# Kernel optimization log

Hardware: AMD Instinct MI355X
Metric: run time of the kernel (lower is better)

## Reference

```python
import jax, jax.numpy as jnp
import numpy as np

DIM, NH, T_MAX = 1024, 16, 2048
HD = DIM // NH
EPS = 1e-6


def _rope_tables(T, hd, dtype=jnp.float32):
    inv_freq = 1.0 / (10000.0 ** (jnp.arange(0, hd, 2, dtype=jnp.float32) / hd))
    t = jnp.arange(T, dtype=jnp.float32)
    freqs = jnp.outer(t, inv_freq)                 # [T, hd/2]
    emb = jnp.concatenate([freqs, freqs], axis=-1)  # [T, hd]
    return jnp.cos(emb).astype(dtype), jnp.sin(emb).astype(dtype)


def _rotate_half(x):
    x1, x2 = jnp.split(x, 2, axis=-1)
    return jnp.concatenate([-x2, x1], axis=-1)


def _rmsnorm(x, g):
    rms = jnp.sqrt(jnp.mean(x * x, axis=-1, keepdims=True) + EPS)
    return x / rms * g


def setup_inputs() -> dict:
    key = jax.random.key(0)
    ks = jax.random.split(key, 10)
    B, T, C = 4, 2048, DIM
    s = 1.0 / np.sqrt(C)
    x = jax.random.normal(ks[0], (B, T, C), dtype=jnp.float32)
    mask = jnp.tril(jnp.ones((T, T), dtype=jnp.int32))[None, None, :, :]
    wq = jax.random.normal(ks[1], (C, C), jnp.float32) * s
    wk = jax.random.normal(ks[2], (C, C), jnp.float32) * s
    wv = jax.random.normal(ks[3], (C, C), jnp.float32) * s
    wo = jax.random.normal(ks[4], (C, C), jnp.float32) * s
    w1 = jax.random.normal(ks[5], (C, 4 * C), jnp.float32) * s
    w2 = jax.random.normal(ks[6], (4 * C, C), jnp.float32) * (1.0 / np.sqrt(4 * C))
    w3 = jax.random.normal(ks[7], (C, 4 * C), jnp.float32) * s
    g1 = jnp.ones((C,), jnp.float32)
    g2 = jnp.ones((C,), jnp.float32)
    return {"x": x, "mask": mask, "g1": g1, "wq": wq, "wk": wk, "wv": wv,
            "wo": wo, "g2": g2, "w1": w1, "w2": w2, "w3": w3}


def reference(x, mask, g1, wq, wk, wv, wo, g2, w1, w2, w3):
    B, T, C = x.shape
    scale = HD ** -0.5
    # --- attention sublayer ---
    h = _rmsnorm(x, g1)
    q = (h @ wq).reshape(B, T, NH, HD)
    k = (h @ wk).reshape(B, T, NH, HD)
    v = (h @ wv).reshape(B, T, NH, HD)
    cos, sin = _rope_tables(T, HD, x.dtype)
    cos = cos[None, :, None, :]
    sin = sin[None, :, None, :]
    q = q * cos + _rotate_half(q) * sin
    k = k * cos + _rotate_half(k) * sin
    attn = jnp.einsum("bthd,bshd->bhts", q, k) * scale  # [B,H,T,T]
    attn = jnp.where(mask == 0, -jnp.inf, attn)
    attn = jax.nn.softmax(attn, axis=-1)
    o = jnp.einsum("bhts,bshd->bthd", attn, v).reshape(B, T, C)
    x = x + o @ wo
    # --- SwiGLU FFN sublayer ---
    h = _rmsnorm(x, g2)
    x = x + (jax.nn.silu(h @ w1) * (h @ w3)) @ w2
    return x
```

## Files before the change

kernel.cpp:

```cpp
#include <hip/hip_runtime.h>
#include <cstdint>

typedef unsigned short u16;
typedef __attribute__((ext_vector_type(8))) short bf16x8;
typedef __attribute__((ext_vector_type(4))) float f32x4;

__device__ __forceinline__ u16 f2b(float f) {
  union { float f; unsigned u; } c; c.f = f;
  unsigned u = c.u;
  return (u16)((u + 0x7FFFu + ((u >> 16) & 1u)) >> 16);
}
__device__ __forceinline__ float b2f(u16 b) {
  union { unsigned u; float f; } c; c.u = ((unsigned)b) << 16;
  return c.f;
}

typedef __attribute__((address_space(1))) void gv_t;
typedef __attribute__((address_space(3))) void lv_t;
__device__ __forceinline__ void gload_lds16(const void* g, void* l) {
  __builtin_amdgcn_global_load_lds((gv_t*)g, (lv_t*)l, 16, 0, 0);
}

__global__ void transpose_f2b(const float* __restrict__ in, u16* __restrict__ out,
                              int R, int C) {
  __shared__ float t[32][33];
  const int c0 = blockIdx.x * 32, r0 = blockIdx.y * 32;
  const int tx = threadIdx.x, ty = threadIdx.y;
#pragma unroll
  for (int i = 0; i < 4; ++i)
    t[ty + 8 * i][tx] = in[(size_t)(r0 + ty + 8 * i) * C + c0 + tx];
  __syncthreads();
#pragma unroll
  for (int i = 0; i < 4; ++i)
    out[(size_t)(c0 + ty + 8 * i) * R + r0 + tx] = f2b(t[tx][ty + 8 * i]);
}

__global__ __launch_bounds__(256) void rmsnorm_k(const float* __restrict__ x,
                                                 const float* __restrict__ g,
                                                 u16* __restrict__ out) {
  const int row = blockIdx.x, tid = threadIdx.x;
  const float4 v = ((const float4*)x)[(size_t)row * 256 + tid];
  float ss = v.x * v.x + v.y * v.y + v.z * v.z + v.w * v.w;
#pragma unroll
  for (int off = 1; off < 64; off <<= 1) ss += __shfl_xor(ss, off, 64);
  __shared__ float red[4];
  if ((tid & 63) == 0) red[tid >> 6] = ss;
  __syncthreads();
  const float mean = (red[0] + red[1] + red[2] + red[3]) * (1.0f / 1024.0f);
  const float rinv = 1.0f / sqrtf(mean + 1e-6f);
  const float4 gv = ((const float4*)g)[tid];
  u16* o = out + (size_t)row * 1024 + tid * 4;
  o[0] = f2b(v.x * rinv * gv.x);
  o[1] = f2b(v.y * rinv * gv.y);
  o[2] = f2b(v.z * rinv * gv.z);
  o[3] = f2b(v.w * rinv * gv.w);
}

__global__ __launch_bounds__(256) void rope_k(u16* __restrict__ qkv) {
  const int i = blockIdx.x * 256 + threadIdx.x;
  const int d = i & 31;
  const int h = (i >> 5) & 15;
  const int bt = i >> 9;
  const int t = bt & 2047;
  const float inv = exp2f((float)d * -0.4152410118609203f);
  const float th = (float)t * inv;
  float s, c;
  sincosf(th, &s, &c);
  size_t base = (size_t)bt * 3072 + h * 64 + d;
#pragma unroll
  for (int half = 0; half < 2; ++half) {
    const float x1 = b2f(qkv[base]);
    const float x2 = b2f(qkv[base + 32]);
    qkv[base]      = f2b(x1 * c - x2 * s);
    qkv[base + 32] = f2b(x2 * c + x1 * s);
    base += 1024;
  }
}

__global__ void vtrans_k(const u16* __restrict__ qkv, u16* __restrict__ VT) {
  __shared__ u16 tl[32][34];
  const int t0 = blockIdx.x * 32;
  const int bh = blockIdx.y >> 1;
  const int d0 = (blockIdx.y & 1) * 32;
  const int b = bh >> 4, h = bh & 15;
  const int tx = threadIdx.x, ty = threadIdx.y;
  const u16* src = qkv + (size_t)(b * 2048 + t0) * 3072 + 2048 + h * 64 + d0;
#pragma unroll
  for (int i = 0; i < 4; ++i)
    tl[ty + 8 * i][tx] = src[(size_t)(ty + 8 * i) * 3072 + tx];
  __syncthreads();
  u16* dst = VT + ((size_t)bh * 64 + d0) * 2048 + t0;
#pragma unroll
  for (int i = 0; i < 4; ++i)
    dst[(size_t)(ty + 8 * i) * 2048 + tx] = tl[tx][ty + 8 * i];
}

template <int EPI>
__global__ __launch_bounds__(512, 2)
void gemm256(const u16* __restrict__ A, const u16* __restrict__ BT,
             void* __restrict__ Cout, const float* __restrict__ resid,
             int M, int N, int K, int lda) {
  __shared__ alignas(16) u16 LDS[65536];
  char* const ldsc = (char*)LDS;
  const int tid = threadIdx.x;
  const int wave = tid >> 6, lane = tid & 63;
  const int wr = wave >> 2, wc = wave & 3;
  const int l15 = lane & 15, quad = lane >> 4;
  const int bm = blockIdx.x * 256, bn = blockIdx.y * 256;
  const int NT = K >> 6;

  const int swz = (l15 & 8) << 2;
  const int aoff = (((wr * 64 + l15) * 64 + quad * 16) ^ swz);
  const int boff = (((wc * 32 + l15) * 64 + quad * 16) ^ swz) + 65536;

  const int kperm = ((lane & 3) ^ ((lane >> 5) << 1)) * 8;
  const u16* sA = A + (size_t)(bm + wave * 16 + (lane >> 2)) * lda + kperm;
  const u16* sB = BT + (size_t)(bn + wave * 16 + (lane >> 2)) * K + kperm;
  const size_t hA = (size_t)128 * lda;
  const size_t hB = (size_t)128 * K;
  const int dstW = wave * 1024;

  f32x4 acc[8][4];
#pragma unroll
  for (int m = 0; m < 8; ++m)
#pragma unroll
    for (int n = 0; n < 4; ++n) acc[m][n] = (f32x4){0.f, 0.f, 0.f, 0.f};
  bf16x8 a[4][2], b[4][2];

#define STAGE(kt_, slot_, buf_)                                               \
  if ((kt_) < NT) {                                                           \
    const u16* s_ = (((slot_) & 1) ? sB + ((size_t)((slot_) >> 1)) * hB       \
                                   : sA + ((size_t)((slot_) >> 1)) * hA) +    \
                    (size_t)(kt_) * 64;                                       \
    char* d_ = ldsc + (((slot_) & 1) ? 65536 : 0) + (buf_) * 32768 +          \
               ((slot_) >> 1) * 16384 + dstW;                                 \
    gload_lds16(s_, d_);                                                      \
    gload_lds16(s_ + 32, d_ + 8192);                                          \
  }

#define LOAD_A(mh_, buf_)                                                     \
  _Pragma("unroll") for (int mf = 0; mf < 4; ++mf)                            \
      _Pragma("unroll") for (int kk = 0; kk < 2; ++kk)                        \
          a[mf][kk] = *(const bf16x8*)(ldsc + aoff + (buf_) * 32768 +         \
                                       (mh_) * 16384 + kk * 8192 + mf * 1024);

#define LOAD_B2(buf_)                                                         \
  _Pragma("unroll") for (int nh = 0; nh < 2; ++nh)                            \
      _Pragma("unroll") for (int nf = 0; nf < 2; ++nf)                        \
          _Pragma("unroll") for (int kk = 0; kk < 2; ++kk)                    \
              b[nh * 2 + nf][kk] =                                            \
                  *(const bf16x8*)(ldsc + boff + (buf_) * 32768 +             \
                                   nh * 16384 + kk * 8192 + nf * 1024);

#define MMA2(mh_)                                                             \
  __builtin_amdgcn_s_setprio(1);                                              \
  _Pragma("unroll") for (int mf = 0; mf < 4; ++mf)                            \
      _Pragma("unroll") for (int n = 0; n < 4; ++n)                           \
          _Pragma("unroll") for (int kk = 0; kk < 2; ++kk)                    \
              acc[(mh_) * 4 + mf][n] =                                        \
                  __builtin_amdgcn_mfma_f32_16x16x32_bf16(                    \
                      a[mf][kk], b[n][kk], acc[(mh_) * 4 + mf][n], 0, 0, 0);  \
  __builtin_amdgcn_s_setprio(0);

#define BAR() __builtin_amdgcn_s_barrier()
#define DRAIN_LGKM()                                                          \
  {                                                                           \
    asm volatile("s_waitcnt lgkmcnt(0)" ::: "memory");                        \
    __builtin_amdgcn_sched_barrier(0);                                        \
  }

  STAGE(0, 0, 0); STAGE(0, 1, 0); STAGE(0, 3, 0);
  STAGE(0, 2, 0);
  STAGE(1, 0, 1); STAGE(1, 1, 1); STAGE(1, 3, 1);
  asm volatile("s_waitcnt vmcnt(8)" ::: "memory");
  BAR();

  for (int t = 0; t < NT; ++t) {
    const int bsel = t & 1;
    LOAD_A(0, bsel); LOAD_B2(bsel);
    STAGE(t + 1, 2, bsel ^ 1);
    BAR(); DRAIN_LGKM(); MMA2(0);
    if (t == NT - 1) { asm volatile("s_waitcnt vmcnt(0)" ::: "memory"); }
    else             { asm volatile("s_waitcnt vmcnt(8)" ::: "memory"); }
    BAR();
    LOAD_A(1, bsel);
    STAGE(t + 2, 0, bsel); STAGE(t + 2, 1, bsel); STAGE(t + 2, 3, bsel);
    BAR(); DRAIN_LGKM(); MMA2(1);
    if (t < NT - 2) {
      asm volatile("s_waitcnt vmcnt(8)" ::: "memory");
      BAR();
    } else if (t == NT - 2) {
      asm volatile("s_waitcnt vmcnt(2)" ::: "memory");
      BAR();
    }
  }
#undef STAGE
#undef LOAD_A
#undef LOAD_B2
#undef MMA2

#pragma unroll
  for (int m = 0; m < 8; ++m) {
    const int gr = bm + (m >> 2) * 128 + wr * 64 + (m & 3) * 16 + quad * 4;
#pragma unroll
    for (int n = 0; n < 4; ++n) {
      const int gc = bn + (n >> 1) * 128 + wc * 32 + (n & 1) * 16 + l15;
#pragma unroll
      for (int r = 0; r < 4; ++r) {
        const size_t off = (size_t)(gr + r) * N + gc;
        if (EPI == 0) {
          ((u16*)Cout)[off] = f2b(acc[m][n][r]);
        } else {
          ((float*)Cout)[off] = resid[off] + acc[m][n][r];
        }
      }
    }
  }
#undef BAR
#undef DRAIN_LGKM
}

__global__ __launch_bounds__(512, 2)
void gemm256g(const u16* __restrict__ A, const u16* __restrict__ B1T,
              const u16* __restrict__ B3T, u16* __restrict__ Cout,
              int Ncols, int K, int lda) {
  __shared__ alignas(16) u16 LDS[65536];
  char* const ldsc = (char*)LDS;
  const int tid = threadIdx.x;
  const int wave = tid >> 6, lane = tid & 63;
  const int wr = wave >> 2, wc = wave & 3;
  const int l15 = lane & 15, quad = lane >> 4;
  const int bm = blockIdx.x * 256, bn = blockIdx.y * 128;
  const int NT = K >> 6;

  const int swz = (l15 & 8) << 2;
  const int aoff  = (((wr * 64 + l15) * 64 + quad * 16) ^ swz);
  const int b1off = (((wc * 32 + l15) * 64 + quad * 16) ^ swz) + 65536;

  const int kperm = ((lane & 3) ^ ((lane >> 5) << 1)) * 8;
  const u16* sA  = A   + (size_t)(bm + wave * 16 + (lane >> 2)) * lda + kperm;
  const u16* sB1 = B1T + (size_t)(bn + wave * 16 + (lane >> 2)) * K + kperm;
  const u16* sB3 = B3T + (size_t)(bn + wave * 16 + (lane >> 2)) * K + kperm;
  const size_t hA = (size_t)128 * lda;
  const int dstW = wave * 1024;

  f32x4 acc1[8][2], acc3[8][2];
#pragma unroll
  for (int m = 0; m < 8; ++m)
#pragma unroll
    for (int n = 0; n < 2; ++n) {
      acc1[m][n] = (f32x4){0.f, 0.f, 0.f, 0.f};
      acc3[m][n] = (f32x4){0.f, 0.f, 0.f, 0.f};
    }
  bf16x8 a[4][2], b1[2][2], b3[2][2];

#define STAGE_A(kt_, half_, buf_)                                             \
  if ((kt_) < NT) {                                                           \
    const u16* s_ = sA + (size_t)(half_) * hA + (size_t)(kt_) * 64;           \
    char* d_ = ldsc + (buf_) * 32768 + (half_) * 16384 + dstW;                \
    gload_lds16(s_, d_);                                                      \
    gload_lds16(s_ + 32, d_ + 8192);                                          \
  }
#define STAGE_B1(kt_, buf_)                                                   \
  if ((kt_) < NT) {                                                           \
    const u16* s_ = sB1 + (size_t)(kt_) * 64;                                 \
    char* d_ = ldsc + 65536 + (buf_) * 16384 + dstW;                          \
    gload_lds16(s_, d_);                                                      \
    gload_lds16(s_ + 32, d_ + 8192);                                          \
  }
#define STAGE_B3(kt_, buf_)                                                   \
  if ((kt_) < NT) {                                                           \
    const u16* s_ = sB3 + (size_t)(kt_) * 64;                                 \
    char* d_ = ldsc + 98304 + (buf_) * 16384 + dstW;                          \
    gload_lds16(s_, d_);                                                      \
    gload_lds16(s_ + 32, d_ + 8192);                                          \
  }
#define LOAD_A(mh_, buf_)                                                     \
  _Pragma("unroll") for (int mf = 0; mf < 4; ++mf)                            \
      _Pragma("unroll") for (int kk = 0; kk < 2; ++kk)                        \
          a[mf][kk] = *(const bf16x8*)(ldsc + aoff + (buf_) * 32768 +         \
                                       (mh_) * 16384 + kk * 8192 + mf * 1024);
#define LOAD_B13(buf_)                                                        \
  _Pragma("unroll") for (int nf = 0; nf < 2; ++nf)                            \
      _Pragma("unroll") for (int kk = 0; kk < 2; ++kk) {                      \
        b1[nf][kk] = *(const bf16x8*)(ldsc + b1off + (buf_) * 16384 +         \
                                      kk * 8192 + nf * 1024);                 \
        b3[nf][kk] = *(const bf16x8*)(ldsc + b1off + 32768 +                  \
                                      (buf_) * 16384 + kk * 8192 +            \
                                      nf * 1024);                             \
      }
#define MMAG(mh_)                                                             \
  __builtin_amdgcn_s_setprio(1);                                              \
  _Pragma("unroll") for (int mf = 0; mf < 4; ++mf)                            \
      _Pragma("unroll") for (int nf = 0; nf < 2; ++nf)                        \
          _Pragma("unroll") for (int kk = 0; kk < 2; ++kk) {                  \
            acc1[(mh_) * 4 + mf][nf] =                                        \
                __builtin_amdgcn_mfma_f32_16x16x32_bf16(                      \
                    a[mf][kk], b1[nf][kk], acc1[(mh_) * 4 + mf][nf], 0, 0, 0);\
            acc3[(mh_) * 4 + mf][nf] =                                        \
                __builtin_amdgcn_mfma_f32_16x16x32_bf16(                      \
                    a[mf][kk], b3[nf][kk], acc3[(mh_) * 4 + mf][nf], 0, 0, 0);\
          }                                                                   \
  __builtin_amdgcn_s_setprio(0);
#define BAR() __builtin_amdgcn_s_barrier()
#define DRAIN_LGKM()                                                          \
  {                                                                           \
    asm volatile("s_waitcnt lgkmcnt(0)" ::: "memory");                        \
    __builtin_amdgcn_sched_barrier(0);                                        \
  }

  STAGE_A(0, 0, 0); STAGE_B1(0, 0); STAGE_B3(0, 0);
  STAGE_A(0, 1, 0);
  STAGE_A(1, 0, 1); STAGE_B1(1, 1); STAGE_B3(1, 1);
  asm volatile("s_waitcnt vmcnt(8)" ::: "memory");
  BAR();

  for (int t = 0; t < NT; ++t) {
    const int bsel = t & 1;
    LOAD_A(0, bsel); LOAD_B13(bsel);
    STAGE_A(t + 1, 1, bsel ^ 1);
    BAR(); DRAIN_LGKM(); MMAG(0);
    if (t == NT - 1) { asm volatile("s_waitcnt vmcnt(0)" ::: "memory"); }
    else             { asm volatile("s_waitcnt vmcnt(8)" ::: "memory"); }
    BAR();
    LOAD_A(1, bsel);
    STAGE_A(t + 2, 0, bsel); STAGE_B1(t + 2, bsel); STAGE_B3(t + 2, bsel);
    BAR(); DRAIN_LGKM(); MMAG(1);
    if (t < NT - 2) {
      asm volatile("s_waitcnt vmcnt(8)" ::: "memory");
      BAR();
    } else if (t == NT - 2) {
      asm volatile("s_waitcnt vmcnt(2)" ::: "memory");
      BAR();
    }
  }
#undef STAGE_A
#undef STAGE_B1
#undef STAGE_B3
#undef LOAD_A
#undef LOAD_B13
#undef MMAG
#undef BAR
#undef DRAIN_LGKM

#pragma unroll
  for (int m = 0; m < 8; ++m) {
    const int gr = bm + (m >> 2) * 128 + wr * 64 + (m & 3) * 16 + quad * 4;
#pragma unroll
    for (int n = 0; n < 2; ++n) {
      const int gc = bn + wc * 32 + n * 16 + l15;
#pragma unroll
      for (int r = 0; r < 4; ++r) {
        const float v1 = acc1[m][n][r];
        const float v3 = acc3[m][n][r];
        const float s = v1 / (1.f + __expf(-v1));
        Cout[(size_t)(gr + r) * Ncols + gc] = f2b(s * v3);
      }
    }
  }
}

template <int EPI>
__global__ __launch_bounds__(512, 2)
void gemm256n(const u16* __restrict__ A, const u16* __restrict__ BT,
              void* __restrict__ Cout, const float* __restrict__ resid,
              int M, int N, int K, int lda) {
  __shared__ alignas(16) u16 LDS[49152];
  char* const ldsc = (char*)LDS;
  const int tid = threadIdx.x;
  const int wave = tid >> 6, lane = tid & 63;
  const int wr = wave >> 2, wc = wave & 3;
  const int l15 = lane & 15, quad = lane >> 4;
  const int bm = blockIdx.x * 256, bn = blockIdx.y * 128;
  const int NT = K >> 6;

  const int swz = (l15 & 8) << 2;
  const int aoff = (((wr * 64 + l15) * 64 + quad * 16) ^ swz);
  const int boff = (((wc * 32 + l15) * 64 + quad * 16) ^ swz) + 65536;

  const int kperm = ((lane & 3) ^ ((lane >> 5) << 1)) * 8;
  const u16* sA = A + (size_t)(bm + wave * 16 + (lane >> 2)) * lda + kperm;
  const u16* sB = BT + (size_t)(bn + wave * 16 + (lane >> 2)) * K + kperm;
  const size_t hA = (size_t)128 * lda;
  const int dstW = wave * 1024;

  f32x4 acc[8][2];
#pragma unroll
  for (int m = 0; m < 8; ++m)
#pragma unroll
    for (int n = 0; n < 2; ++n) acc[m][n] = (f32x4){0.f, 0.f, 0.f, 0.f};
  bf16x8 a[4][2], b[2][2];

#define STAGE_A(kt_, half_, buf_)                                             \
  if ((kt_) < NT) {                                                           \
    const u16* s_ = sA + (size_t)(half_) * hA + (size_t)(kt_) * 64;           \
    char* d_ = ldsc + (buf_) * 32768 + (half_) * 16384 + dstW;                \
    gload_lds16(s_, d_);                                                      \
    gload_lds16(s_ + 32, d_ + 8192);                                          \
  }
#define STAGE_B(kt_, buf_)                                                    \
  if ((kt_) < NT) {                                                           \
    const u16* s_ = sB + (size_t)(kt_) * 64;                                  \
    char* d_ = ldsc + 65536 + (buf_) * 16384 + dstW;                          \
    gload_lds16(s_, d_);                                                      \
    gload_lds16(s_ + 32, d_ + 8192);                                          \
  }
#define LOAD_A(mh_, buf_)                                                     \
  _Pragma("unroll") for (int mf = 0; mf < 4; ++mf)                            \
      _Pragma("unroll") for (int kk = 0; kk < 2; ++kk)                        \
          a[mf][kk] = *(const bf16x8*)(ldsc + aoff + (buf_) * 32768 +         \
                                       (mh_) * 16384 + kk * 8192 + mf * 1024);
#define LOAD_B(buf_)                                                          \
  _Pragma("unroll") for (int nf = 0; nf < 2; ++nf)                            \
      _Pragma("unroll") for (int kk = 0; kk < 2; ++kk)                        \
          b[nf][kk] = *(const bf16x8*)(ldsc + boff + (buf_) * 16384 +         \
                                       kk * 8192 + nf * 1024);
#define MMA(mh_)                                                              \
  __builtin_amdgcn_s_setprio(1);                                              \
  _Pragma("unroll") for (int mf = 0; mf < 4; ++mf)                            \
      _Pragma("unroll") for (int nf = 0; nf < 2; ++nf)                        \
          _Pragma("unroll") for (int kk = 0; kk < 2; ++kk)                    \
              acc[(mh_) * 4 + mf][nf] =                                       \
                  __builtin_amdgcn_mfma_f32_16x16x32_bf16(                    \
                      a[mf][kk], b[nf][kk], acc[(mh_) * 4 + mf][nf], 0, 0, 0);\
  __builtin_amdgcn_s_setprio(0);
#define BAR() __builtin_amdgcn_s_barrier()
#define DRAIN_LGKM()                                                          \
  {                                                                           \
    asm volatile("s_waitcnt lgkmcnt(0)" ::: "memory");                        \
    __builtin_amdgcn_sched_barrier(0);                                        \
  }

  STAGE_A(0, 0, 0); STAGE_B(0, 0);
  STAGE_A(0, 1, 0);
  STAGE_A(1, 0, 1); STAGE_B(1, 1);
  asm volatile("s_waitcnt vmcnt(6)" ::: "memory");
  BAR();

  for (int t = 0; t < NT; ++t) {
    const int bsel = t & 1;
    LOAD_A(0, bsel); LOAD_B(bsel);
    STAGE_A(t + 1, 1, bsel ^ 1);
    BAR(); DRAIN_LGKM(); MMA(0);
    if (t == NT - 1) { asm volatile("s_waitcnt vmcnt(0)" ::: "memory"); }
    else             { asm volatile("s_waitcnt vmcnt(6)" ::: "memory"); }
    BAR();
    LOAD_A(1, bsel);
    STAGE_A(t + 2, 0, bsel); STAGE_B(t + 2, bsel);
    BAR(); DRAIN_LGKM(); MMA(1);
    if (t == NT - 2)     { asm volatile("s_waitcnt vmcnt(2)" ::: "memory"); }
    else if (t < NT - 2) { asm volatile("s_waitcnt vmcnt(6)" ::: "memory"); }
    BAR();
  }
#undef STAGE_A
#undef STAGE_B
#undef LOAD_A
#undef LOAD_B
#undef MMA
#undef BAR
#undef DRAIN_LGKM

#pragma unroll
  for (int m = 0; m < 8; ++m) {
    const int gr = bm + (m >> 2) * 128 + wr * 64 + (m & 3) * 16 + quad * 4;
#pragma unroll
    for (int n = 0; n < 2; ++n) {
      const int gc = bn + wc * 32 + n * 16 + l15;
#pragma unroll
      for (int r = 0; r < 4; ++r) {
        const size_t off = (size_t)(gr + r) * N + gc;
        if (EPI == 0) {
          ((u16*)Cout)[off] = f2b(acc[m][n][r]);
        } else {
          ((float*)Cout)[off] = resid[off] + acc[m][n][r];
        }
      }
    }
  }
}

__global__ __launch_bounds__(256)
void attn_kernel(const u16* __restrict__ QKV, const u16* __restrict__ VT,
                 u16* __restrict__ O, float* __restrict__ Opart,
                 float* __restrict__ Spart) {
  const int T = 2048, stQ = 3072;
  const int tid = threadIdx.x, wave = tid >> 6, lane = tid & 63;
  const int l15 = lane & 15, quad = lane >> 4;

  const int xi = (int)blockIdx.x;
  const bool split = (xi < 22);
  const int qt = split ? (15 - (xi >> 1)) : (26 - xi);
  const int chunk = split ? (xi & 1) : 0;
  const int len = split ? (qt + 1) : (2 * qt + 2);
  const int kt0 = chunk * (qt + 1);
  const int ktEnd = kt0 + len;

  const int qb0 = qt * 128;
  const int bh = blockIdx.y, b = bh >> 4, h = bh & 15;
  const float sc2 = 0.125f * 1.44269504088896f;
  const float M0 = 32.0f;

  __shared__ alignas(16) u16 Kf[2][8 * 512];
  __shared__ alignas(16) u16 Vf[2][8 * 512];
  __shared__ alignas(16) u16 Pl[4][2][16 * 72];

  const u16* Qb  = QKV + (size_t)b * T * stQ + h * 64;
  const u16* Kb  = Qb + 1024;
  const u16* VTb = VT + (size_t)bh * 64 * T;

  const int r0 = qb0 + wave * 16;
  const int r1 = r0 + 64;
  const u16* qp0 = Qb + (size_t)(r0 + l15) * stQ + quad * 8;
  const u16* qp1 = Qb + (size_t)(r1 + l15) * stQ + quad * 8;
  const bf16x8 qf00 = *(const bf16x8*)qp0;
  const bf16x8 qf01 = *(const bf16x8*)(qp0 + 32);
  const bf16x8 qf10 = *(const bf16x8*)qp1;
  const bf16x8 qf11 = *(const bf16x8*)(qp1 + 32);

  bf16x8 ones;
#pragma unroll
  for (int j = 0; j < 8; ++j) ones[j] = (short)0x3F80;

  const u16* kS = Kb + (size_t)(wave * 16 + l15) * stQ + quad * 8;
  const u16* vS = VTb + (size_t)(wave * 16 + l15) * T + quad * 8;

  f32x4 o0[4], o1[4], sum0, sum1;
#pragma unroll
  for (int c = 0; c < 4; ++c) {
    o0[c] = (f32x4){0.f, 0.f, 0.f, 0.f};
    o1[c] = (f32x4){0.f, 0.f, 0.f, 0.f};
  }
  sum0 = (f32x4){0.f, 0.f, 0.f, 0.f};
  sum1 = (f32x4){0.f, 0.f, 0.f, 0.f};

  u16* pw0 = &Pl[wave][0][0];
  u16* pw1 = &Pl[wave][1][0];

  gload_lds16(kS + (size_t)(kt0 * 64) * stQ,      &Kf[0][(wave * 2 + 0) * 512]);
  gload_lds16(kS + (size_t)(kt0 * 64) * stQ + 32, &Kf[0][(wave * 2 + 1) * 512]);
  gload_lds16(vS + (size_t)(kt0 * 64),            &Vf[0][(wave * 2 + 0) * 512]);
  gload_lds16(vS + (size_t)(kt0 * 64) + 32,       &Vf[0][(wave * 2 + 1) * 512]);

  for (int kt = kt0; kt < ktEnd; ++kt) {
    const int kb0 = kt * 64;
    const int buf = (kt - kt0) & 1;
    __builtin_amdgcn_sched_barrier(0);
    if (kt + 1 < ktEnd) {
      const size_t kb1 = (size_t)(kb0 + 64);
      gload_lds16(kS + kb1 * stQ,      &Kf[buf ^ 1][(wave * 2 + 0) * 512]);
      gload_lds16(kS + kb1 * stQ + 32, &Kf[buf ^ 1][(wave * 2 + 1) * 512]);
      gload_lds16(vS + kb1,            &Vf[buf ^ 1][(wave * 2 + 0) * 512]);
      gload_lds16(vS + kb1 + 32,       &Vf[buf ^ 1][(wave * 2 + 1) * 512]);
      asm volatile("s_waitcnt vmcnt(4)" ::: "memory");
    } else {
      asm volatile("s_waitcnt vmcnt(0)" ::: "memory");
    }
    __builtin_amdgcn_s_barrier();
    __builtin_amdgcn_sched_barrier(0);

    bf16x8 kf[8], vf[8];
#pragma unroll
    for (int g = 0; g < 8; ++g) {
      kf[g] = *(const bf16x8*)(&Kf[buf][g * 512 + lane * 8]);
      vf[g] = *(const bf16x8*)(&Vf[buf][g * 512 + lane * 8]);
    }

    const bool act0 = (kb0 <= r0 + 15);

    {
      f32x4 s[4];
      __builtin_amdgcn_s_setprio(1);
#pragma unroll
      for (int jj = 0; jj < 4; ++jj) {
        s[jj] = (f32x4){0.f, 0.f, 0.f, 0.f};
        s[jj] = __builtin_amdgcn_mfma_f32_16x16x32_bf16(qf10, kf[jj * 2 + 0], s[jj], 0, 0, 0);
        s[jj] = __builtin_amdgcn_mfma_f32_16x16x32_bf16(qf11, kf[jj * 2 + 1], s[jj], 0, 0, 0);
      }
      __builtin_amdgcn_s_setprio(0);
      if (kb0 + 63 > r1) {
#pragma unroll
        for (int jj = 0; jj < 4; ++jj)
#pragma unroll
          for (int r = 0; r < 4; ++r) {
            const bool msk = (kb0 + jj * 16 + l15) > (r1 + quad * 4 + r);
            const float a = msk ? -1e30f : (s[jj][r] * sc2 - M0);
            pw1[(quad * 4 + r) * 72 + jj * 16 + l15] = f2b(exp2f(a));
          }
      } else {
#pragma unroll
        for (int jj = 0; jj < 4; ++jj)
#pragma unroll
          for (int r = 0; r < 4; ++r)
            pw1[(quad * 4 + r) * 72 + jj * 16 + l15] =
                f2b(exp2f(s[jj][r] * sc2 - M0));
      }
    }
    if (act0) {
      f32x4 s[4];
      __builtin_amdgcn_s_setprio(1);
#pragma unroll
      for (int jj = 0; jj < 4; ++jj) {
        s[jj] = (f32x4){0.f, 0.f, 0.f, 0.f};
        s[jj] = __builtin_amdgcn_mfma_f32_16x16x32_bf16(qf00, kf[jj * 2 + 0], s[jj], 0, 0, 0);
        s[jj] = __builtin_amdgcn_mfma_f32_16x16x32_bf16(qf01, kf[jj * 2 + 1], s[jj], 0, 0, 0);
      }
      __builtin_amdgcn_s_setprio(0);
      if (kb0 + 63 > r0) {
#pragma unroll
        for (int jj = 0; jj < 4; ++jj)
#pragma unroll
          for (int r = 0; r < 4; ++r) {
            const bool msk = (kb0 + jj * 16 + l15) > (r0 + quad * 4 + r);
            const float a = msk ? -1e30f : (s[jj][r] * sc2 - M0);
            pw0[(quad * 4 + r) * 72 + jj * 16 + l15] = f2b(exp2f(a));
          }
      } else {
#pragma unroll
        for (int jj = 0; jj < 4; ++jj)
#pragma unroll
          for (int r = 0; r < 4; ++r)
            pw0[(quad * 4 + r) * 72 + jj * 16 + l15] =
                f2b(exp2f(s[jj][r] * sc2 - M0));
      }
    }

    const bf16x8 pf10 = *(const bf16x8*)(pw1 + l15 * 72 + quad * 8);
    const bf16x8 pf11 = *(const bf16x8*)(pw1 + l15 * 72 + 32 + quad * 8);
    __builtin_amdgcn_s_setprio(1);
#pragma unroll
    for (int c = 0; c < 4; ++c) {
      o1[c] = __builtin_amdgcn_mfma_f32_16x16x32_bf16(pf10, vf[c * 2 + 0], o1[c], 0, 0, 0);
      o1[c] = __builtin_amdgcn_mfma_f32_16x16x32_bf16(pf11, vf[c * 2 + 1], o1[c], 0, 0, 0);
    }
    sum1 = __builtin_amdgcn_mfma_f32_16x16x32_bf16(pf10, ones, sum1, 0, 0, 0);
    sum1 = __builtin_amdgcn_mfma_f32_16x16x32_bf16(pf11, ones, sum1, 0, 0, 0);
    __builtin_amdgcn_s_setprio(0);
    if (act0) {
      const bf16x8 pf00 = *(const bf16x8*)(pw0 + l15 * 72 + quad * 8);
      const bf16x8 pf01 = *(const bf16x8*)(pw0 + l15 * 72 + 32 + quad * 8);
      __builtin_amdgcn_s_setprio(1);
#pragma unroll
      for (int c = 0; c < 4; ++c) {
        o0[c] = __builtin_amdgcn_mfma_f32_16x16x32_bf16(pf00, vf[c * 2 + 0], o0[c], 0, 0, 0);
        o0[c] = __builtin_amdgcn_mfma_f32_16x16x32_bf16(pf01, vf[c * 2 + 1], o0[c], 0, 0, 0);
      }
      sum0 = __builtin_amdgcn_mfma_f32_16x16x32_bf16(pf00, ones, sum0, 0, 0, 0);
      sum0 = __builtin_amdgcn_mfma_f32_16x16x32_bf16(pf01, ones, sum0, 0, 0, 0);
      __builtin_amdgcn_s_setprio(0);
    }
    __builtin_amdgcn_s_barrier();
  }

  if (split) {
    const int pi = (bh * 11 + (qt - 5)) * 2 + chunk;
    float* Po = Opart + (size_t)pi * 8192;
    float* Ps = Spart + (size_t)pi * 128;
    const int lr0 = wave * 16 + quad * 4;
#pragma unroll
    for (int c = 0; c < 4; ++c)
#pragma unroll
      for (int r = 0; r < 4; ++r) {
        Po[(lr0 + r) * 64 + c * 16 + l15]      = o0[c][r];
        Po[(64 + lr0 + r) * 64 + c * 16 + l15] = o1[c][r];
      }
    if (l15 == 0) {
#pragma unroll
      for (int r = 0; r < 4; ++r) {
        Ps[lr0 + r]      = sum0[r];
        Ps[64 + lr0 + r] = sum1[r];
      }
    }
  } else {
    float i0[4], i1[4];
#pragma unroll
    for (int r = 0; r < 4; ++r) { i0[r] = 1.f / sum0[r]; i1[r] = 1.f / sum1[r]; }
    u16* op0 = O + ((size_t)(b * T) + r0 + quad * 4) * 1024 + h * 64 + l15;
    u16* op1 = O + ((size_t)(b * T) + r1 + quad * 4) * 1024 + h * 64 + l15;
#pragma unroll
    for (int c = 0; c < 4; ++c)
#pragma unroll
      for (int r = 0; r < 4; ++r) {
        op0[(size_t)r * 1024 + c * 16] = f2b(o0[c][r] * i0[r]);
        op1[(size_t)r * 1024 + c * 16] = f2b(o1[c][r] * i1[r]);
      }
  }
}

__global__ __launch_bounds__(256)
void attn_combine(const float* __restrict__ Opart, const float* __restrict__ Spart,
                  u16* __restrict__ O) {
  const int sp = blockIdx.x;
  const int bh = sp / 11, qt = 5 + (sp % 11);
  const int b = bh >> 4, h = bh & 15;
  const int t = threadIdx.x;
  const int row = t >> 1, ch = (t & 1) * 32;
  const size_t p0 = (size_t)(2 * sp) * 8192, p1 = p0 + 8192;
  const float s = Spart[(size_t)(2 * sp) * 128 + row] +
                  Spart[(size_t)(2 * sp) * 128 + 128 + row];
  const float inv = 1.f / s;
  const float4* A  = (const float4*)(Opart + p0 + row * 64 + ch);
  const float4* Bv = (const float4*)(Opart + p1 + row * 64 + ch);
  u16* op = O + ((size_t)(b * 2048) + qt * 128 + row) * 1024 + h * 64 + ch;
#pragma unroll
  for (int j = 0; j < 8; ++j) {
    const float4 a = A[j], bb = Bv[j];
    op[j * 4 + 0] = f2b((a.x + bb.x) * inv);
    op[j * 4 + 1] = f2b((a.y + bb.y) * inv);
    op[j * 4 + 2] = f2b((a.z + bb.z) * inv);
    op[j * 4 + 3] = f2b((a.w + bb.w) * inv);
  }
}

extern "C" void kernel_launch(void* const* d_in, const int* in_sizes, int n_in,
                              void* d_out, int out_size, void* d_ws, size_t ws_size,
                              hipStream_t stream) {
  const float* x  = (const float*)d_in[0];
  const float* g1 = (const float*)d_in[2];
  const float* wq = (const float*)d_in[3];
  const float* wk = (const float*)d_in[4];
  const float* wv = (const float*)d_in[5];
  const float* wo = (const float*)d_in[6];
  const float* g2 = (const float*)d_in[7];
  const float* w1 = (const float*)d_in[8];
  const float* w2 = (const float*)d_in[9];
  const float* w3 = (const float*)d_in[10];
  float* out = (float*)d_out;

  const int T = 2048, NH = 16, B = 4;
  const int M = B * T;
  const size_t MB = 1ull << 20;

  char* ws = (char*)d_ws;
  u16* hb    = (u16*)(ws);
  u16* wqkvT = (u16*)(ws + 16 * MB);
  u16* woT   = (u16*)(ws + 22 * MB);
  u16* w13T  = (u16*)(ws + 24 * MB);
  u16* w2T   = (u16*)(ws + 40 * MB);
  u16* qkv   = (u16*)(ws + 48 * MB);
  u16* VT    = (u16*)(ws + 96 * MB);
  u16* Ob    = (u16*)(ws + 112 * MB);
  u16* a13g  = (u16*)(ws + 48 * MB);
  float* Opart = (float*)(ws + 128 * MB);
  float* Spart = Opart + (size_t)1408 * 8192;

  const dim3 tb(32, 8);
  transpose_f2b<<<dim3(32, 32),  tb, 0, stream>>>(wq, wqkvT,              1024, 1024);
  transpose_f2b<<<dim3(32, 32),  tb, 0, stream>>>(wk, wqkvT + 1024*1024,  1024, 1024);
  transpose_f2b<<<dim3(32, 32),  tb, 0, stream>>>(wv, wqkvT + 2048*1024,  1024, 1024);
  transpose_f2b<<<dim3(32, 32),  tb, 0, stream>>>(wo, woT, 1024, 1024);
  transpose_f2b<<<dim3(128, 32), tb, 0, stream>>>(w1, w13T,               1024, 4096);
  transpose_f2b<<<dim3(128, 32), tb, 0, stream>>>(w3, w13T + 4096*1024,   1024, 4096);
  transpose_f2b<<<dim3(32, 128), tb, 0, stream>>>(w2, w2T, 4096, 1024);

  rmsnorm_k<<<M, 256, 0, stream>>>(x, g1, hb);

  gemm256<0><<<dim3(32, 12), 512, 0, stream>>>(hb, wqkvT, qkv, nullptr, M, 3072, 1024, 1024);

  rope_k<<<16384, 256, 0, stream>>>(qkv);
  vtrans_k<<<dim3(64, 128), tb, 0, stream>>>(qkv, VT);

  attn_kernel<<<dim3(27, B * NH), 256, 0, stream>>>(qkv, VT, Ob, Opart, Spart);
  attn_combine<<<dim3(704), 256, 0, stream>>>(Opart, Spart, Ob);

  gemm256n<1><<<dim3(32, 8), 512, 0, stream>>>(Ob, woT, out, x, M, 1024, 1024, 1024);

  rmsnorm_k<<<M, 256, 0, stream>>>(out, g2, hb);

  gemm256g<<<dim3(32, 32), 512, 0, stream>>>(hb, w13T, w13T + (size_t)4096 * 1024,
                                             a13g, 4096, 1024, 1024);

  gemm256n<1><<<dim3(32, 8), 512, 0, stream>>>(a13g, w2T, out, out, M, 1024, 4096, 4096);
}
```

Measured before the change: 637.7 us.

## Remap gemm256n waves to a 4x2 grid of 64x64 tiles with single-phase loads

Changes the wave layout in the 256x128 GEMM from a 2x4 grid (each wave covering 128x32 in two halves) to a 4x2 grid where each wave owns a 64x64 sub-tile. Each wave now loads all its A and B fragments from LDS once per k-step, and the pipeline stages the whole next tile in one phase instead of two. The aim is fewer LDS fragment reads per MFMA, since a square per-wave tile reuses operands better, plus fewer barriers per iteration. In exchange it holds more B fragments in registers and changes when global-to-LDS prefetch overlaps with compute, which could expose load latency or add register pressure.

```diff
diff --git a/kernel.cpp b/kernel.cpp
--- a/kernel.cpp
+++ b/kernel.cpp
@@ -369,14 +369,15 @@
   char* const ldsc = (char*)LDS;
   const int tid = threadIdx.x;
   const int wave = tid >> 6, lane = tid & 63;
-  const int wr = wave >> 2, wc = wave & 3;
+  const int wr = wave >> 1, wc = wave & 1;
   const int l15 = lane & 15, quad = lane >> 4;
   const int bm = blockIdx.x * 256, bn = blockIdx.y * 128;
   const int NT = K >> 6;
 
   const int swz = (l15 & 8) << 2;
-  const int aoff = (((wr * 64 + l15) * 64 + quad * 16) ^ swz);
-  const int boff = (((wc * 32 + l15) * 64 + quad * 16) ^ swz) + 65536;
+  const int aoff = (wr >> 1) * 16384 +
+                   ((((wr & 1) * 64 + l15) * 64 + quad * 16) ^ swz);
+  const int boff = (((wc * 64 + l15) * 64 + quad * 16) ^ swz) + 65536;
 
   const int kperm = ((lane & 3) ^ ((lane >> 5) << 1)) * 8;
   const u16* sA = A + (size_t)(bm + wave * 16 + (lane >> 2)) * lda + kperm;
@@ -384,12 +385,12 @@
   const size_t hA = (size_t)128 * lda;
   const int dstW = wave * 1024;
 
-  f32x4 acc[8][2];
-#pragma unroll
-  for (int m = 0; m < 8; ++m)
-#pragma unroll
-    for (int n = 0; n < 2; ++n) acc[m][n] = (f32x4){0.f, 0.f, 0.f, 0.f};
-  bf16x8 a[4][2], b[2][2];
+  f32x4 acc[4][4];
+#pragma unroll
+  for (int m = 0; m < 4; ++m)
+#pragma unroll
+    for (int n = 0; n < 4; ++n) acc[m][n] = (f32x4){0.f, 0.f, 0.f, 0.f};
+  bf16x8 a[4][2], b[4][2];
 
 #define STAGE_A(kt_, half_, buf_)                                             \
   if ((kt_) < NT) {                                                           \
@@ -405,24 +406,24 @@
     gload_lds16(s_, d_);                                                      \
     gload_lds16(s_ + 32, d_ + 8192);                                          \
   }
-#define LOAD_A(mh_, buf_)                                                     \
+#define LOAD_ALL(buf_)                                                        \
   _Pragma("unroll") for (int mf = 0; mf < 4; ++mf)                            \
       _Pragma("unroll") for (int kk = 0; kk < 2; ++kk)                        \
           a[mf][kk] = *(const bf16x8*)(ldsc + aoff + (buf_) * 32768 +         \
-                                       (mh_) * 16384 + kk * 8192 + mf * 1024);
-#define LOAD_B(buf_)                                                          \
-  _Pragma("unroll") for (int nf = 0; nf < 2; ++nf)                            \
+                                       kk * 8192 + mf * 1024);                \
+  _Pragma("unroll") for (int nf = 0; nf < 4; ++nf)                            \
       _Pragma("unroll") for (int kk = 0; kk < 2; ++kk)                        \
           b[nf][kk] = *(const bf16x8*)(ldsc + boff + (buf_) * 16384 +         \
                                        kk * 8192 + nf * 1024);
-#define MMA(mh_)                                                              \
+#define MMA_N(nlo_)                                                           \
   __builtin_amdgcn_s_setprio(1);                                              \
   _Pragma("unroll") for (int mf = 0; mf < 4; ++mf)                            \
       _Pragma("unroll") for (int nf = 0; nf < 2; ++nf)                        \
           _Pragma("unroll") for (int kk = 0; kk < 2; ++kk)                    \
-              acc[(mh_) * 4 + mf][nf] =                                       \
+              acc[mf][(nlo_) * 2 + nf] =                                      \
                   __builtin_amdgcn_mfma_f32_16x16x32_bf16(                    \
-                      a[mf][kk], b[nf][kk], acc[(mh_) * 4 + mf][nf], 0, 0, 0);\
+                      a[mf][kk], b[(nlo_) * 2 + nf][kk],                      \
+                      acc[mf][(nlo_) * 2 + nf], 0, 0, 0);                     \
   __builtin_amdgcn_s_setprio(0);
 #define BAR() __builtin_amdgcn_s_barrier()
 #define DRAIN_LGKM()                                                          \
@@ -431,41 +432,40 @@
     __builtin_amdgcn_sched_barrier(0);                                        \
   }
 
-  STAGE_A(0, 0, 0); STAGE_B(0, 0);
-  STAGE_A(0, 1, 0);
-  STAGE_A(1, 0, 1); STAGE_B(1, 1);
+  STAGE_A(0, 0, 0); STAGE_A(0, 1, 0); STAGE_B(0, 0);
+  STAGE_A(1, 0, 1); STAGE_A(1, 1, 1); STAGE_B(1, 1);
   asm volatile("s_waitcnt vmcnt(6)" ::: "memory");
   BAR();
 
   for (int t = 0; t < NT; ++t) {
     const int bsel = t & 1;
-    LOAD_A(0, bsel); LOAD_B(bsel);
-    STAGE_A(t + 1, 1, bsel ^ 1);
-    BAR(); DRAIN_LGKM(); MMA(0);
-    if (t == NT - 1) { asm volatile("s_waitcnt vmcnt(0)" ::: "memory"); }
-    else             { asm volatile("s_waitcnt vmcnt(6)" ::: "memory"); }
+    LOAD_ALL(bsel);
+    BAR(); DRAIN_LGKM();
+    MMA_N(0);
     BAR();
-    LOAD_A(1, bsel);
-    STAGE_A(t + 2, 0, bsel); STAGE_B(t + 2, bsel);
-    BAR(); DRAIN_LGKM(); MMA(1);
-    if (t == NT - 2)     { asm volatile("s_waitcnt vmcnt(2)" ::: "memory"); }
-    else if (t < NT - 2) { asm volatile("s_waitcnt vmcnt(6)" ::: "memory"); }
-    BAR();
+    STAGE_A(t + 2, 0, bsel); STAGE_A(t + 2, 1, bsel); STAGE_B(t + 2, bsel);
+    MMA_N(1);
+    if (t + 2 < NT) {
+      asm volatile("s_waitcnt vmcnt(6)" ::: "memory");
+      BAR();
+    } else if (t + 1 < NT) {
+      asm volatile("s_waitcnt vmcnt(0)" ::: "memory");
+      BAR();
+    }
   }
 #undef STAGE_A
 #undef STAGE_B
-#undef LOAD_A
-#undef LOAD_B
-#undef MMA
+#undef LOAD_ALL
+#undef MMA_N
 #undef BAR
 #undef DRAIN_LGKM
 
 #pragma unroll
-  for (int m = 0; m < 8; ++m) {
-    const int gr = bm + (m >> 2) * 128 + wr * 64 + (m & 3) * 16 + quad * 4;
-#pragma unroll
-    for (int n = 0; n < 2; ++n) {
-      const int gc = bn + wc * 32 + n * 16 + l15;
+  for (int m = 0; m < 4; ++m) {
+    const int gr = bm + wr * 64 + m * 16 + quad * 4;
+#pragma unroll
+    for (int n = 0; n < 4; ++n) {
+      const int gc = bn + wc * 64 + n * 16 + l15;
 #pragma unroll
       for (int r = 0; r < 4; ++r) {
         const size_t off = (size_t)(gr + r) * N + gc;
```

Result: no change. 637.9 us (+0.0%).
